# Optimization experiments

Measured on AMD Instinct MI355X. Metric: run time of the kernel, lower is better.

## Reference

```python
import jax, jax.numpy as jnp
import numpy as np


def setup_inputs() -> dict:
    key = jax.random.key(0)
    ks = jax.random.split(key, 8)
    B, N, K, C_in, M, C_add, C_out = 2, 40000, 16, 64, 16, 3, 128
    in_features = (C_in + C_add) * M  # 1072
    input_features = jax.random.normal(ks[0], (B, N, C_in), dtype=jnp.float32)
    neighbor_inds = jax.random.randint(ks[1], (B, N, K), 0, N, dtype=jnp.int64)
    inverse_neighbors = jax.random.randint(ks[2], (B, N * K), 0, N * K, dtype=jnp.int64)
    inverse_k = jax.random.randint(ks[3], (B, N * K), 0, K, dtype=jnp.int64)
    inverse_idx = jax.random.randint(ks[4], (B, N * K), 0, N, dtype=jnp.int64)
    weightnet = jax.random.normal(ks[5], (B, N, K, M), dtype=jnp.float32)
    additional_features = jax.random.normal(ks[6], (B, N, K, C_add), dtype=jnp.float32)
    bound = 1.0 / np.sqrt(in_features)
    kw, kb = jax.random.split(ks[7])
    linear_weight = jax.random.uniform(kw, (C_out, in_features), dtype=jnp.float32, minval=-bound, maxval=bound)
    linear_bias = jax.random.uniform(kb, (C_out,), dtype=jnp.float32, minval=-bound, maxval=bound)
    return {
        "input_features": input_features,
        "neighbor_inds": neighbor_inds,
        "inverse_neighbors": inverse_neighbors,
        "inverse_k": inverse_k,
        "inverse_idx": inverse_idx,
        "weightnet": weightnet,
        "additional_features": additional_features,
        "linear_weight": linear_weight,
        "linear_bias": linear_bias,
    }


def reference(input_features, neighbor_inds, inverse_neighbors, inverse_k, inverse_idx,
              weightnet, additional_features, linear_weight, linear_bias):
    # inverse_* tensors are only used by the custom CUDA backward; unused here.
    B, N, K = neighbor_inds.shape
    # gather neighbor features: [B, N, K, C_in]
    gathered = jnp.take_along_axis(input_features[:, :, None, :],
                                   neighbor_inds[..., None], axis=1)
    # concat extra per-neighbor features -> [B, N, K, C]
    feats = jnp.concatenate([gathered, additional_features], axis=-1)
    # PConv: [B,N,C,K] @ [B,N,K,M] -> [B,N,C,M] -> flatten to [B,N,C*M]
    pconv = jnp.einsum('bnkc,bnkm->bncm', feats, weightnet)
    pconv = pconv.reshape(B, N, -1)
    # fused linear
    out = jnp.einsum('bnf,of->bno', pconv, linear_weight) + linear_bias
    return out
```

## Files before the change

kernel.cpp:

```cpp
#include <hip/hip_runtime.h>
#include <stdint.h>

typedef unsigned short u16;
typedef short short8 __attribute__((ext_vector_type(8)));
typedef float floatx4 __attribute__((ext_vector_type(4)));

#define NPERB   40000
#define NPTS    80000
#define KNBR    16
#define CIN     64
#define MDIM    16
#define CADD    3
#define CF      (CIN + CADD)
#define COUT    128
#define KF      1072
#define KP      1088
#define NKT     34
#define PTSB    16
#define SLAB    65

__device__ __forceinline__ u16 f2bf(float f) {
    union { float f; unsigned int u; } v; v.f = f;
    unsigned int u = v.u;
    return (u16)((u + 0x7FFFu + ((u >> 16) & 1u)) >> 16);
}
__device__ __forceinline__ short8 pack8(floatx4 x, floatx4 y) {
    union { short8 v; u16 a[8]; } u;
    u.a[0] = f2bf(x[0]); u.a[1] = f2bf(x[1]); u.a[2] = f2bf(x[2]); u.a[3] = f2bf(x[3]);
    u.a[4] = f2bf(y[0]); u.a[5] = f2bf(y[1]); u.a[6] = f2bf(y[2]); u.a[7] = f2bf(y[3]);
    return u.v;
}
__device__ __forceinline__ unsigned swz(unsigned chunk) {
    return chunk ^ ((chunk >> 3) & 7u);
}
__device__ __forceinline__ void gload_lds16(const void* g, void* l) {
    __builtin_amdgcn_global_load_lds(
        (const __attribute__((address_space(1))) void*)g,
        (__attribute__((address_space(3))) void*)l, 16, 0, 0);
}

__global__ void prep_lw_kernel(const float* __restrict__ lw, u16* __restrict__ lwp) {
    int i = blockIdx.x * 256 + threadIdx.x;
    if (i >= COUT * KP) return;
    int o = i / KP, f = i - o * KP;
    lwp[i] = (f < KF) ? f2bf(lw[(size_t)o * KF + f]) : (u16)0;
}

__device__ __forceinline__ void compute_point(
    int pr, int lane, float av, const float (&fv)[KNBR],
    const float* wl, u16* Apc)
{
    const int em = lane & 15, ec = lane >> 4;
    float ev = 0.f;
#pragma unroll
    for (int k = 0; k < KNBR; k++)
        ev += __shfl(av, k * CADD + ec) * wl[k * MDIM + em];
    if (ec == 3) ev = 0.f;
    {
        unsigned kt   = 32 + (lane >> 5);
        unsigned quad = (lane >> 3) & 3;
        unsigned ch   = kt * SLAB + (unsigned)pr * 4 + quad;
        Apc[swz(ch) * 8 + (lane & 7)] = f2bf(ev);
    }
    floatx4 a0 = 0, a1 = 0, a2 = 0, a3 = 0;
#pragma unroll
    for (int k = 0; k < KNBR; k++) {
        const floatx4* w4 = (const floatx4*)(wl + k * MDIM);
        const float fvk = fv[k];
        a0 += fvk * w4[0]; a1 += fvk * w4[1];
        a2 += fvk * w4[2]; a3 += fvk * w4[3];
    }
    {
        unsigned kt = lane >> 1, qb = (lane & 1) * 2;
        unsigned ch = kt * SLAB + (unsigned)pr * 4 + qb;
        *(short8*)&Apc[swz(ch) * 8]     = pack8(a0, a1);
        *(short8*)&Apc[swz(ch + 1) * 8] = pack8(a2, a3);
    }
}

__global__ __launch_bounds__(512, 6) void fused_kernel(
    const float* __restrict__ inp,
    const int*   __restrict__ nbr,
    const float* __restrict__ wn,
    const float* __restrict__ addl,
    const u16*   __restrict__ lwp,
    const float* __restrict__ bias,
    float* __restrict__ out)
{
    __shared__ __align__(16) u16   Apc[(NKT * SLAB + 8) * 8];
    __shared__ __align__(16) float Wns[PTSB * KNBR * MDIM];

    const int wave = threadIdx.x >> 6;
    const int lane = threadIdx.x & 63;
    const int pbase = blockIdx.x * PTSB;
    const float* inpb = inp + ((pbase >= NPERB) ? (size_t)NPERB * CIN : 0);

    const int pr0 = wave * 2;
    const int p0  = __builtin_amdgcn_readfirstlane(pbase + pr0);
    const int p1  = p0 + 1;

    float* wl0 = Wns + pr0 * (KNBR * MDIM);
    float* wl1 = wl0 + KNBR * MDIM;
    gload_lds16(wn + (size_t)p0 * (KNBR * MDIM) + lane * 4, wl0);
    gload_lds16(wn + (size_t)p1 * (KNBR * MDIM) + lane * 4, wl1);

    float av0 = (lane < KNBR * CADD) ? addl[(size_t)p0 * (KNBR * CADD) + lane] : 0.f;
    float av1 = (lane < KNBR * CADD) ? addl[(size_t)p1 * (KNBR * CADD) + lane] : 0.f;

    const int* nb0 = nbr + (size_t)p0 * KNBR;
    const int* nb1 = nbr + (size_t)p1 * KNBR;
    int idx0[KNBR], idx1[KNBR];
#pragma unroll
    for (int k = 0; k < KNBR; k++) idx0[k] = nb0[k];
#pragma unroll
    for (int k = 0; k < KNBR; k++) idx1[k] = nb1[k];

    float fv0[KNBR], fv1[KNBR];
#pragma unroll
    for (int k = 0; k < KNBR; k++) fv0[k] = inpb[(size_t)idx0[k] * CIN + lane];
#pragma unroll
    for (int k = 0; k < KNBR; k++) fv1[k] = inpb[(size_t)idx1[k] * CIN + lane];

    asm volatile("s_waitcnt vmcnt(0)" ::: "memory");
    __builtin_amdgcn_sched_barrier(0);

    compute_point(pr0,     lane, av0, fv0, wl0, Apc);
    compute_point(pr0 + 1, lane, av1, fv1, wl1, Apc);

    const int r16 = lane & 15, quad = lane >> 4;
    const int c0 = wave * 16;
    const u16* Bp = lwp + (size_t)(c0 + r16) * KP + quad * 8;
    const unsigned abase = (unsigned)r16 * 4 + quad;
    const float bv = bias[c0 + r16];

    __syncthreads();

    floatx4 acc = 0;
#pragma unroll 2
    for (int kt = 0; kt < NKT; kt++) {
        short8 A = *(const short8*)&Apc[swz((unsigned)kt * SLAB + abase) * 8];
        short8 B = *(const short8*)(Bp + kt * 32);
        acc = __builtin_amdgcn_mfma_f32_16x16x32_bf16(A, B, acc, 0, 0, 0);
    }

#pragma unroll
    for (int r = 0; r < 4; r++) {
        const size_t row = (size_t)(pbase + quad * 4 + r) * COUT;
        out[row + c0 + r16] = acc[r] + bv;
    }
}

__global__ __launch_bounds__(256) void fused_fallback_kernel(
    const float* __restrict__ inp, const int* __restrict__ nbr,
    const float* __restrict__ wn, const float* __restrict__ addl,
    const float* __restrict__ lw, const float* __restrict__ bias,
    float* __restrict__ out)
{
    const int p = blockIdx.x;
    const int b = p / NPERB;
    const int tid = threadIdx.x;
    __shared__ float sf[KNBR * CF];
    __shared__ float sw[KNBR * MDIM];
    __shared__ float sp[KF];

    sw[tid] = wn[(size_t)p * (KNBR * MDIM) + tid];
    for (int i = tid; i < KNBR * CIN; i += 256) {
        int k = i >> 6, c = i & 63;
        int idx = nbr[(size_t)p * KNBR + k];
        sf[k * CF + c] = inp[((size_t)b * NPERB + idx) * CIN + c];
    }
    if (tid < KNBR * CADD) {
        int k = tid / CADD, c = tid - k * CADD;
        sf[k * CF + CIN + c] = addl[(size_t)p * (KNBR * CADD) + tid];
    }
    __syncthreads();
    for (int f = tid; f < KF; f += 256) {
        int c = f >> 4, m = f & 15;
        float s = 0;
#pragma unroll
        for (int k = 0; k < KNBR; k++) s += sf[k * CF + c] * sw[k * MDIM + m];
        sp[f] = s;
    }
    __syncthreads();
    const int o = tid >> 1, h = tid & 1;
    float s = 0;
    for (int f = h * (KF / 2); f < (h + 1) * (KF / 2); f++)
        s += sp[f] * lw[(size_t)o * KF + f];
    s += __shfl_xor(s, 1);
    if (h == 0) out[(size_t)p * COUT + o] = s + bias[o];
}

extern "C" void kernel_launch(void* const* d_in, const int* in_sizes, int n_in,
                              void* d_out, int out_size, void* d_ws, size_t ws_size,
                              hipStream_t stream) {
    const float* inp  = (const float*)d_in[0];
    const int*   nbr  = (const int*)d_in[1];
    const float* wn   = (const float*)d_in[5];
    const float* addl = (const float*)d_in[6];
    const float* lw   = (const float*)d_in[7];
    const float* bias = (const float*)d_in[8];
    float* out = (float*)d_out;

    const size_t lw_bytes = (size_t)COUT * KP * sizeof(u16);
    if (ws_size < lw_bytes) {
        fused_fallback_kernel<<<NPTS, 256, 0, stream>>>(inp, nbr, wn, addl, lw, bias, out);
        return;
    }
    u16* lwp = (u16*)d_ws;
    prep_lw_kernel<<<(COUT * KP + 255) / 256, 256, 0, stream>>>(lw, lwp);
    fused_kernel<<<NPTS / PTSB, 512, 0, stream>>>(inp, nbr, wn, addl, lwp, bias, out);
}
```

Measured before the change: 378.0 us.

## Split fused kernel into pconv kernel and tiled bf16 GEMM via workspace

Unfuses the point-convolution and linear stages: a first kernel writes per-point bf16 pconv features to a workspace buffer, then a separate GEMM kernel processes 64-point tiles with double-buffered LDS loads of A and four MFMA accumulators per wave. This aims to improve weight reuse and MFMA utilization in the linear stage. In exchange it adds a large intermediate write and read through global memory. The split path only runs if the workspace is big enough; otherwise it falls back to the old fused path.

```diff
diff --git a/kernel.cpp b/kernel.cpp
--- a/kernel.cpp
+++ b/kernel.cpp
@@ -18,6 +18,8 @@
 #define NKT     34
 #define PTSB    16
 #define SLAB    65
+#define GR      64
+#define PPB     8
 
 __device__ __forceinline__ u16 f2bf(float f) {
     union { float f; unsigned int u; } v; v.f = f;
@@ -33,6 +35,9 @@
 __device__ __forceinline__ unsigned swz(unsigned chunk) {
     return chunk ^ ((chunk >> 3) & 7u);
 }
+__device__ __forceinline__ unsigned aswz(unsigned c) {
+    return c ^ ((c >> 4) & 3u);
+}
 __device__ __forceinline__ void gload_lds16(const void* g, void* l) {
     __builtin_amdgcn_global_load_lds(
         (const __attribute__((address_space(1))) void*)g,
@@ -44,6 +49,147 @@
     if (i >= COUT * KP) return;
     int o = i / KP, f = i - o * KP;
     lwp[i] = (f < KF) ? f2bf(lw[(size_t)o * KF + f]) : (u16)0;
+}
+
+__device__ __forceinline__ void emit_point(
+    int lane, float av, const float (&fv)[KNBR], const float* wl,
+    u16* __restrict__ dst)
+{
+    const int em = lane & 15, ec = lane >> 4;
+    float ev = 0.f;
+#pragma unroll
+    for (int k = 0; k < KNBR; k++)
+        ev += __shfl(av, k * CADD + ec) * wl[k * MDIM + em];
+    if (ec == 3) ev = 0.f;
+    dst[1024 + lane] = f2bf(ev);
+
+    floatx4 a0 = 0, a1 = 0, a2 = 0, a3 = 0;
+#pragma unroll
+    for (int k = 0; k < KNBR; k++) {
+        const floatx4* w4 = (const floatx4*)(wl + k * MDIM);
+        const float fvk = fv[k];
+        a0 += fvk * w4[0]; a1 += fvk * w4[1];
+        a2 += fvk * w4[2]; a3 += fvk * w4[3];
+    }
+    *(short8*)(dst + lane * 16)     = pack8(a0, a1);
+    *(short8*)(dst + lane * 16 + 8) = pack8(a2, a3);
+}
+
+__global__ __launch_bounds__(256) void pconv_kernel(
+    const float* __restrict__ inp,
+    const int*   __restrict__ nbr,
+    const float* __restrict__ wn,
+    const float* __restrict__ addl,
+    u16* __restrict__ pc)
+{
+    __shared__ __align__(16) float Wns[PPB * KNBR * MDIM];
+
+    const int wave = threadIdx.x >> 6;
+    const int lane = threadIdx.x & 63;
+    const int pbase = blockIdx.x * PPB;
+    const float* inpb = inp + ((pbase >= NPERB) ? (size_t)NPERB * CIN : 0);
+
+    const int pr0 = wave * 2;
+    const int p0  = __builtin_amdgcn_readfirstlane(pbase + pr0);
+    const int p1  = p0 + 1;
+
+    float* wl0 = Wns + pr0 * (KNBR * MDIM);
+    float* wl1 = wl0 + KNBR * MDIM;
+    gload_lds16(wn + (size_t)p0 * (KNBR * MDIM) + lane * 4, wl0);
+    gload_lds16(wn + (size_t)p1 * (KNBR * MDIM) + lane * 4, wl1);
+
+    float av0 = (lane < KNBR * CADD) ? addl[(size_t)p0 * (KNBR * CADD) + lane] : 0.f;
+    float av1 = (lane < KNBR * CADD) ? addl[(size_t)p1 * (KNBR * CADD) + lane] : 0.f;
+
+    const int* nb0 = nbr + (size_t)p0 * KNBR;
+    const int* nb1 = nbr + (size_t)p1 * KNBR;
+    int idx0[KNBR], idx1[KNBR];
+#pragma unroll
+    for (int k = 0; k < KNBR; k++) idx0[k] = nb0[k];
+#pragma unroll
+    for (int k = 0; k < KNBR; k++) idx1[k] = nb1[k];
+
+    float fv0[KNBR], fv1[KNBR];
+#pragma unroll
+    for (int k = 0; k < KNBR; k++) fv0[k] = inpb[(size_t)idx0[k] * CIN + lane];
+#pragma unroll
+    for (int k = 0; k < KNBR; k++) fv1[k] = inpb[(size_t)idx1[k] * CIN + lane];
+
+    asm volatile("s_waitcnt vmcnt(0)" ::: "memory");
+    __builtin_amdgcn_sched_barrier(0);
+
+    emit_point(lane, av0, fv0, wl0, pc + (size_t)p0 * KP);
+    emit_point(lane, av1, fv1, wl1, pc + (size_t)p1 * KP);
+}
+
+__global__ __launch_bounds__(512) void gemm_kernel(
+    const u16* __restrict__ pc,
+    const u16* __restrict__ lwp,
+    const float* __restrict__ bias,
+    float* __restrict__ out)
+{
+    __shared__ __align__(16) u16 At[2][GR * 32];
+
+    const int wave = threadIdx.x >> 6;
+    const int lane = threadIdx.x & 63;
+    const int pbase = blockIdx.x * GR;
+    const int r16 = lane & 15, quad = lane >> 4;
+    const int rt = wave & 3;
+    const int c0 = (wave >> 2) * 64;
+
+    const u16* ssrc = nullptr;
+    if (wave < 4) {
+        unsigned s = (unsigned)wave * 64 + lane;
+        unsigned c = aswz(s);
+        ssrc = pc + (size_t)(pbase + (c >> 2)) * KP + (c & 3u) * 8;
+    }
+    u16* sdst0 = &At[0][(size_t)wave * 64 * 8];
+    u16* sdst1 = &At[1][(size_t)wave * 64 * 8];
+
+    const unsigned ca = (unsigned)(rt * 16 + r16) * 4 + quad;
+    const unsigned slot = aswz(ca);
+
+    const u16* B0 = lwp + (size_t)(c0 + r16) * KP + quad * 8;
+    const u16* B1 = B0 + (size_t)16 * KP;
+    const u16* B2 = B0 + (size_t)32 * KP;
+    const u16* B3 = B0 + (size_t)48 * KP;
+    const float bv0 = bias[c0 + r16];
+    const float bv1 = bias[c0 + 16 + r16];
+    const float bv2 = bias[c0 + 32 + r16];
+    const float bv3 = bias[c0 + 48 + r16];
+
+    if (wave < 4) gload_lds16(ssrc, sdst0);
+    asm volatile("s_waitcnt vmcnt(0)" ::: "memory");
+    __syncthreads();
+
+    floatx4 acc0 = 0, acc1 = 0, acc2 = 0, acc3 = 0;
+    int cur = 0;
+    for (int kt = 0; kt < NKT; kt++) {
+        if (kt + 1 < NKT && wave < 4)
+            gload_lds16(ssrc + (size_t)(kt + 1) * 32, cur ? sdst0 : sdst1);
+
+        short8 A  = *(const short8*)&At[cur][slot * 8];
+        short8 b0 = *(const short8*)(B0 + kt * 32);
+        short8 b1 = *(const short8*)(B1 + kt * 32);
+        short8 b2 = *(const short8*)(B2 + kt * 32);
+        short8 b3 = *(const short8*)(B3 + kt * 32);
+        acc0 = __builtin_amdgcn_mfma_f32_16x16x32_bf16(A, b0, acc0, 0, 0, 0);
+        acc1 = __builtin_amdgcn_mfma_f32_16x16x32_bf16(A, b1, acc1, 0, 0, 0);
+        acc2 = __builtin_amdgcn_mfma_f32_16x16x32_bf16(A, b2, acc2, 0, 0, 0);
+        acc3 = __builtin_amdgcn_mfma_f32_16x16x32_bf16(A, b3, acc3, 0, 0, 0);
+
+        __syncthreads();
+        cur ^= 1;
+    }
+
+#pragma unroll
+    for (int r = 0; r < 4; r++) {
+        const size_t row = (size_t)(pbase + rt * 16 + quad * 4 + r) * COUT;
+        out[row + c0 + r16]      = acc0[r] + bv0;
+        out[row + c0 + 16 + r16] = acc1[r] + bv1;
+        out[row + c0 + 32 + r16] = acc2[r] + bv2;
+        out[row + c0 + 48 + r16] = acc3[r] + bv3;
+    }
 }
 
 __device__ __forceinline__ void compute_point(
@@ -79,12 +225,9 @@
 }
 
 __global__ __launch_bounds__(512, 6) void fused_kernel(
-    const float* __restrict__ inp,
-    const int*   __restrict__ nbr,
-    const float* __restrict__ wn,
-    const float* __restrict__ addl,
-    const u16*   __restrict__ lwp,
-    const float* __restrict__ bias,
+    const float* __restrict__ inp, const int* __restrict__ nbr,
+    const float* __restrict__ wn, const float* __restrict__ addl,
+    const u16* __restrict__ lwp, const float* __restrict__ bias,
     float* __restrict__ out)
 {
     __shared__ __align__(16) u16   Apc[(NKT * SLAB + 8) * 8];
@@ -202,11 +345,19 @@
     float* out = (float*)d_out;
 
     const size_t lw_bytes = (size_t)COUT * KP * sizeof(u16);
-    if (ws_size < lw_bytes) {
+    const size_t pc_bytes = (size_t)NPTS * KP * sizeof(u16);
+
+    if (ws_size >= lw_bytes + pc_bytes) {
+        u16* lwp = (u16*)d_ws;
+        u16* pcw = lwp + (size_t)COUT * KP;
+        prep_lw_kernel<<<(COUT * KP + 255) / 256, 256, 0, stream>>>(lw, lwp);
+        pconv_kernel<<<NPTS / PPB, 256, 0, stream>>>(inp, nbr, wn, addl, pcw);
+        gemm_kernel<<<NPTS / GR, 512, 0, stream>>>(pcw, lwp, bias, out);
+    } else if (ws_size >= lw_bytes) {
+        u16* lwp = (u16*)d_ws;
+        prep_lw_kernel<<<(COUT * KP + 255) / 256, 256, 0, stream>>>(lw, lwp);
+        fused_kernel<<<NPTS / PTSB, 512, 0, stream>>>(inp, nbr, wn, addl, lwp, bias, out);
+    } else {
         fused_fallback_kernel<<<NPTS, 256, 0, stream>>>(inp, nbr, wn, addl, lw, bias, out);
-        return;
-    }
-    u16* lwp = (u16*)d_ws;
-    prep_lw_kernel<<<(COUT * KP + 255) / 256, 256, 0, stream>>>(lw, lwp);
-    fused_kernel<<<NPTS / PTSB, 512, 0, stream>>>(inp, nbr, wn, addl, lwp, bias, out);
-}
+    }
+}
```

New measurement: 378.4 us. About the same (+0.1%).
